# Kernel tuning notes

Hardware: AMD Instinct MI355X
Metric: run time of the kernel (lower is better)

## Reference

```python
import jax, jax.numpy as jnp
import numpy as np

N_HEADS = 16
N_KV_HEADS = 4
HEAD_DIM = 128  # d_model // n_heads = 2048 // 16
ROPE_THETA = 10000.0


def _rope_cos_sin(T, D, dtype):
    inv_freq = 1.0 / (ROPE_THETA ** (jnp.arange(0, D, 2, dtype=jnp.float32) / D))
    t = jnp.arange(T, dtype=jnp.float32)
    freqs = jnp.outer(t, inv_freq)               # [T, D/2]
    emb = jnp.concatenate([freqs, freqs], axis=-1)  # [T, D]
    return jnp.cos(emb).astype(dtype), jnp.sin(emb).astype(dtype)


def _rotate_half(x):
    x1, x2 = jnp.split(x, 2, axis=-1)
    return jnp.concatenate([-x2, x1], axis=-1)


def setup_inputs() -> dict:
    key = jax.random.key(0)
    k1, k2, k3, k4, k5 = jax.random.split(key, 5)
    B, T, C = 2, 2048, 2048
    H, KV, D = N_HEADS, N_KV_HEADS, HEAD_DIM
    s = 0.02
    return {
        "x": jax.random.normal(k1, (B, T, C), dtype=jnp.float32),
        "Wq": jax.random.normal(k2, (C, H * D), dtype=jnp.float32) * s,
        "Wk": jax.random.normal(k3, (C, KV * D), dtype=jnp.float32) * s,
        "Wv": jax.random.normal(k4, (C, KV * D), dtype=jnp.float32) * s,
        "Wo": jax.random.normal(k5, (H * D, C), dtype=jnp.float32) * s,
    }


def reference(x, Wq, Wk, Wv, Wo):
    B, T, C = x.shape
    H, KV, D = N_HEADS, N_KV_HEADS, HEAD_DIM
    G = H // KV
    scale = D ** -0.5

    q = (x @ Wq).reshape(B, T, H, D).transpose(0, 2, 1, 3)    # [B,H,T,D]
    k = (x @ Wk).reshape(B, T, KV, D).transpose(0, 2, 1, 3)   # [B,KV,T,D]
    v = (x @ Wv).reshape(B, T, KV, D).transpose(0, 2, 1, 3)   # [B,KV,T,D]

    cos, sin = _rope_cos_sin(T, D, x.dtype)  # [T,D] each, broadcasts over B,H
    q = q * cos + _rotate_half(q) * sin
    k = k * cos + _rotate_half(k) * sin

    # repeat_interleave kv heads to match query heads
    k = jnp.repeat(k, G, axis=1)  # [B,H,T,D]
    v = jnp.repeat(v, G, axis=1)  # [B,H,T,D]

    scores = jnp.einsum('bhqd,bhkd->bhqk', q, k) * scale  # [B,H,T,T]
    causal = jnp.tril(jnp.ones((T, T), dtype=bool))
    scores = jnp.where(causal, scores, jnp.finfo(scores.dtype).min)
    attn = jax.nn.softmax(scores, axis=-1)

    out = jnp.einsum('bhqk,bhkd->bhqd', attn, v)           # [B,H,T,D]
    out = out.transpose(0, 2, 1, 3).reshape(B, T, H * D)    # [B,T,C]
    return out @ Wo
```

## Files before the change

kernel.cpp:

```cpp
#include <hip/hip_runtime.h>
#include <cstdint>
#include <cstddef>

typedef __attribute__((ext_vector_type(4))) float f32x4;
typedef __attribute__((ext_vector_type(8))) short s16x8;
typedef __attribute__((ext_vector_type(4))) short s16x4;

#define B_  2
#define T_  2048
#define C_  2048
#define H_  16
#define KV_ 4
#define D_  128
#define M_  4096

static __device__ __forceinline__ float bf2f(ushort u){
  union { float f; uint32_t u; } x; x.u = ((uint32_t)u) << 16; return x.f;
}
static __device__ __forceinline__ ushort f2bf(float f){
  union { float f; uint32_t u; } x; x.f = f;
  uint32_t r = x.u + 0x7FFF + ((x.u >> 16) & 1);
  return (ushort)(r >> 16);
}

static __device__ __forceinline__ void gl_lds16(const ushort* g, ushort* s){
  __builtin_amdgcn_global_load_lds((const __attribute__((address_space(1))) void*)g,
                                   (__attribute__((address_space(3))) void*)s, 16, 0, 0);
}

__global__ void cvt_f32_bf16(const float* __restrict__ in, ushort* __restrict__ out, int n4){
  int idx = blockIdx.x * blockDim.x + threadIdx.x;
  int stride = gridDim.x * blockDim.x;
  for (int i = idx; i < n4; i += stride){
    float4 v = ((const float4*)in)[i];
    s16x4 o;
    o[0] = (short)f2bf(v.x); o[1] = (short)f2bf(v.y);
    o[2] = (short)f2bf(v.z); o[3] = (short)f2bf(v.w);
    ((s16x4*)out)[i] = o;
  }
}

__global__ void transpose_cvt(const float* __restrict__ W, ushort* __restrict__ Wt, int K, int N){
  __shared__ float tile[32][33];
  int n0 = blockIdx.x * 32, k0 = blockIdx.y * 32;
  int tx = threadIdx.x, ty = threadIdx.y;
  #pragma unroll
  for (int r = 0; r < 4; r++)
    tile[ty + 8*r][tx] = W[(size_t)(k0 + ty + 8*r) * N + n0 + tx];
  __syncthreads();
  #pragma unroll
  for (int r = 0; r < 4; r++)
    Wt[(size_t)(n0 + ty + 8*r) * K + k0 + tx] = f2bf(tile[tx][ty + 8*r]);
}

template<int MODE>
__global__ __launch_bounds__(512)
void gemm_deep(const ushort* __restrict__ A, const ushort* __restrict__ Bt,
               void* __restrict__ C0, void* __restrict__ C1, void* __restrict__ C2,
               int N, int Kd, int nbx){
  __shared__ __align__(16) ushort Abuf[4][8192];
  __shared__ __align__(16) ushort Bbuf[4][8192];
  int tid = threadIdx.x, w = tid >> 6, l = tid & 63;
  int l15 = l & 15, l4 = l >> 4;

  int cpx = gridDim.x >> 3;
  int logical = (blockIdx.x & 7) * cpx + (blockIdx.x >> 3);
  int bx = logical % nbx, by = logical / nbx;
  int rblk = by * 128, cblk = bx * 128;
  int wm = w & 1, wn = w >> 1;

  int sr = tid >> 3;
  int sc = ((tid & 7) * 8) ^ ((sr & 7) << 3);
  const ushort* gA = A  + (size_t)(rblk + sr) * Kd + sc;
  const ushort* gB = Bt + (size_t)(cblk + sr) * Kd + sc;
  size_t rowK = (size_t)64 * Kd;
  int wb = w * 512;

  auto stage = [&](int t){
    int bsel = t & 3; int koff = t * 64;
    gl_lds16(gA + koff,        &Abuf[bsel][wb]);
    gl_lds16(gA + rowK + koff, &Abuf[bsel][4096 + wb]);
    gl_lds16(gB + koff,        &Bbuf[bsel][wb]);
    gl_lds16(gB + rowK + koff, &Bbuf[bsel][4096 + wb]);
  };

  int arow = wm * 64 + l15;
  int brow = wn * 32 + l15;
  int kx0 = (l4 * 8) ^ ((l15 & 7) << 3);
  int kx1 = (32 + l4 * 8) ^ ((l15 & 7) << 3);

  f32x4 acc[4][2] = {};

  auto phase = [&](int t, int dostage, int vm){
    const ushort* Ab = Abuf[t & 3];
    const ushort* Bb = Bbuf[t & 3];
    s16x8 a[4][2], b[2][2];
    #pragma unroll
    for (int m = 0; m < 4; m++){
      a[m][0] = *(const s16x8*)(Ab + (arow + m*16) * 64 + kx0);
      a[m][1] = *(const s16x8*)(Ab + (arow + m*16) * 64 + kx1);
    }
    #pragma unroll
    for (int n = 0; n < 2; n++){
      b[n][0] = *(const s16x8*)(Bb + (brow + n*16) * 64 + kx0);
      b[n][1] = *(const s16x8*)(Bb + (brow + n*16) * 64 + kx1);
    }
    if (dostage) stage(t + 3);
    if (vm == 8)      { asm volatile("s_waitcnt vmcnt(8)" ::: "memory"); }
    else if (vm == 4) { asm volatile("s_waitcnt vmcnt(4)" ::: "memory"); }
    else if (vm == 0) { asm volatile("s_waitcnt vmcnt(0)" ::: "memory"); }
    if (vm >= 0) __builtin_amdgcn_sched_barrier(0);
    __builtin_amdgcn_s_barrier();
    asm volatile("s_waitcnt lgkmcnt(0)" ::: "memory");
    __builtin_amdgcn_sched_barrier(0);
    __builtin_amdgcn_s_setprio(1);
    #pragma unroll
    for (int m = 0; m < 4; m++)
      #pragma unroll
      for (int n = 0; n < 2; n++){
        acc[m][n] = __builtin_amdgcn_mfma_f32_16x16x32_bf16(a[m][0], b[n][0], acc[m][n], 0, 0, 0);
        acc[m][n] = __builtin_amdgcn_mfma_f32_16x16x32_bf16(a[m][1], b[n][1], acc[m][n], 0, 0, 0);
      }
    __builtin_amdgcn_s_setprio(0);
    __builtin_amdgcn_s_barrier();
  };

  stage(0); stage(1); stage(2);
  asm volatile("s_waitcnt vmcnt(8)" ::: "memory");
  __builtin_amdgcn_s_barrier();

  int nt = Kd >> 6;
  for (int t = 0; t < nt - 3; ++t) phase(t, 1, 8);
  phase(nt - 3, 0, 4);
  phase(nt - 2, 0, 0);
  phase(nt - 1, 0, -1);

  #pragma unroll
  for (int m = 0; m < 4; m++){
    #pragma unroll
    for (int n = 0; n < 2; n++){
      #pragma unroll
      for (int j = 0; j < 4; j++){
        int row = rblk + wm*64 + m*16 + l4*4 + j;
        int col = cblk + wn*32 + n*16 + l15;
        float v = acc[m][n][j];
        if (MODE == 0){
          ((float*)C0)[(size_t)row * N + col] = v;
        } else {
          int t = row & (T_ - 1), bb = row >> 11;
          ushort bv = f2bf(v);
          if (cblk < 2048){
            int hh = col >> 7, d = col & 127;
            ((ushort*)C0)[(((size_t)(bb * H_ + hh)) * T_ + t) * D_ + d] = bv;
          } else if (cblk < 2560){
            int c2 = col - 2048;
            int hh = c2 >> 7, d = c2 & 127;
            ((ushort*)C1)[(((size_t)(bb * KV_ + hh)) * T_ + t) * D_ + d] = bv;
          } else {
            int c2 = col - 2560;
            int hh = c2 >> 7, d = c2 & 127;
            ((ushort*)C2)[(((size_t)(bb * KV_ + hh)) * D_ + d) * T_ + t] = bv;
          }
        }
      }
    }
  }
}

__global__ __launch_bounds__(256)
void rope_inplace2(ushort* __restrict__ X, float scale){
  int tr = threadIdx.x >> 4;
  int j  = threadIdx.x & 15;
  int t  = blockIdx.x * 16 + tr;
  int bh = blockIdx.y;
  ushort* row = X + ((size_t)bh * T_ + t) * D_;
  s16x4 lo = *(const s16x4*)(row + j*4);
  s16x4 hi = *(const s16x4*)(row + 64 + j*4);
  s16x4 olo, ohi;
  #pragma unroll
  for (int i = 0; i < 4; i++){
    int d = j*4 + i;
    float invf = exp2f(-(float)d * 0.2076205059304602f);
    float s, c;
    __sincosf((float)t * invf, &s, &c);
    float q1 = bf2f((ushort)lo[i]);
    float q2 = bf2f((ushort)hi[i]);
    olo[i] = (short)f2bf((q1 * c - q2 * s) * scale);
    ohi[i] = (short)f2bf((q2 * c + q1 * s) * scale);
  }
  *(s16x4*)(row + j*4) = olo;
  *(s16x4*)(row + 64 + j*4) = ohi;
}

__global__ __launch_bounds__(512, 4)
void attn_kernel4(const ushort* __restrict__ Q, const ushort* __restrict__ Kc,
                  const ushort* __restrict__ Vt, ushort* __restrict__ O){
  __shared__ __align__(16) ushort Ks[64 * 128];
  __shared__ __align__(16) ushort Vs[128 * 64];
  __shared__ __align__(16) ushort Ps[8 * 16 * 64];
  int bid = blockIdx.x;
  int i  = bid >> 3;
  int qt = (i < 32) ? (63 - i) : (i - 32);
  int sub = bid & 7;
  int b = sub >> 2, kvh = sub & 3;
  int tid = threadIdx.x, w = tid >> 6, l = tid & 63;
  int l15 = l & 15, l4 = l >> 4;
  int sw3 = (l15 & 7) << 3;
  int q0 = qt * 32;
  int hq = kvh * 4 + (w >> 1);
  int qrow0 = q0 + (w & 1) * 16;
  int qrow = qrow0 + l15;

  s16x8 qf[4];
  const ushort* qbase = Q + (((size_t)(b * H_ + hq)) * T_ + qrow) * D_;
  #pragma unroll
  for (int kk = 0; kk < 4; kk++)
    qf[kk] = *(const s16x8*)(qbase + kk * 32 + l4 * 8);

  f32x4 oacc[8] = {};
  float mrun = -1e30f;
  float rsum = 0.f;
  const float THR = 11.5415603f;
  ushort* Pw = Ps + w * (16 * 64) + l15 * 64;

  const ushort* kbase = Kc + ((size_t)(b * KV_ + kvh)) * T_ * D_;
  const ushort* vbase = Vt + ((size_t)(b * KV_ + kvh)) * D_ * T_;
  int jmax = (q0 + 31) >> 6;

  int kr0 = tid >> 4, kcb = tid & 15;
  int vd0 = tid >> 3, vtb = tid & 7;
  int ksoff = kr0 * 128 + ((kcb * 8) ^ ((kr0 & 7) << 3));
  int vsoff = vd0 * 64  + ((vtb * 8) ^ ((vd0 & 7) << 3));
  const ushort* kg = kbase + (size_t)kr0 * D_ + kcb * 8;
  const ushort* vg = vbase + (size_t)vd0 * T_ + vtb * 8;

  s16x8 kreg0, kreg1, vreg0, vreg1;
  kreg0 = *(const s16x8*)(kg);
  kreg1 = *(const s16x8*)(kg + (size_t)32 * D_);
  vreg0 = *(const s16x8*)(vg);
  vreg1 = *(const s16x8*)(vg + (size_t)64 * T_);

  for (int jt = 0; jt <= jmax; jt++){
    __syncthreads();
    *(s16x8*)(Ks + ksoff)            = kreg0;
    *(s16x8*)(Ks + ksoff + 32 * 128) = kreg1;
    *(s16x8*)(Vs + vsoff)            = vreg0;
    *(s16x8*)(Vs + vsoff + 64 * 64)  = vreg1;
    __syncthreads();
    if (jt < jmax){
      int k1 = (jt + 1) * 64;
      kreg0 = *(const s16x8*)(kg + (size_t)k1 * D_);
      kreg1 = *(const s16x8*)(kg + (size_t)(k1 + 32) * D_);
      vreg0 = *(const s16x8*)(vg + k1);
      vreg1 = *(const s16x8*)(vg + (size_t)64 * T_ + k1);
    }
    int k0 = jt * 64;

    f32x4 sacc[4] = {};
    __builtin_amdgcn_s_setprio(1);
    #pragma unroll
    for (int kk = 0; kk < 4; kk++){
      #pragma unroll
      for (int n = 0; n < 4; n++){
        s16x8 kf = *(const s16x8*)(Ks + (16*n + l15) * 128 + ((kk*32 + l4*8) ^ sw3));
        sacc[n] = __builtin_amdgcn_mfma_f32_16x16x32_bf16(kf, qf[kk], sacc[n], 0, 0, 0);
      }
    }
    __builtin_amdgcn_s_setprio(0);
    if (jt == jmax){
      #pragma unroll
      for (int n = 0; n < 4; n++)
        #pragma unroll
        for (int j = 0; j < 4; j++){
          int kcol = k0 + 16*n + 4*l4 + j;
          if (kcol > qrow) sacc[n][j] = -1e30f;
        }
    }
    float mloc = -1e30f;
    #pragma unroll
    for (int n = 0; n < 4; n++)
      #pragma unroll
      for (int j = 0; j < 4; j++)
        mloc = fmaxf(mloc, sacc[n][j]);
    if (__any((int)(mloc > mrun + THR))){
      float m2 = fmaxf(mloc, __shfl_xor(mloc, 16));
      m2 = fmaxf(m2, __shfl_xor(m2, 32));
      float mnew = fmaxf(mrun, m2);
      float alpha = exp2f(mrun - mnew);
      mrun = mnew;
      rsum *= alpha;
      #pragma unroll
      for (int n8 = 0; n8 < 8; n8++)
        #pragma unroll
        for (int j = 0; j < 4; j++)
          oacc[n8][j] *= alpha;
    }
    #pragma unroll
    for (int n = 0; n < 4; n++){
      s16x4 pk;
      #pragma unroll
      for (int j = 0; j < 4; j++){
        float p = exp2f(sacc[n][j] - mrun);
        rsum += p;
        pk[j] = (short)f2bf(p);
      }
      *(s16x4*)(Pw + ((16*n + 4*l4) ^ sw3)) = pk;
    }
    __builtin_amdgcn_s_setprio(1);
    #pragma unroll
    for (int kk = 0; kk < 2; kk++){
      s16x8 pf = *(const s16x8*)(Pw + ((kk*32 + l4*8) ^ sw3));
      #pragma unroll
      for (int n8 = 0; n8 < 8; n8++){
        s16x8 vf = *(const s16x8*)(Vs + (16*n8 + l15) * 64 + ((kk*32 + l4*8) ^ sw3));
        oacc[n8] = __builtin_amdgcn_mfma_f32_16x16x32_bf16(vf, pf, oacc[n8], 0, 0, 0);
      }
    }
    __builtin_amdgcn_s_setprio(0);
  }

  rsum += __shfl_xor(rsum, 16);
  rsum += __shfl_xor(rsum, 32);
  float inv = 1.f / rsum;
  ushort* obase = O + ((size_t)(b * T_ + qrow)) * C_ + hq * D_ + 4*l4;
  #pragma unroll
  for (int n8 = 0; n8 < 8; n8++){
    s16x4 ov;
    #pragma unroll
    for (int j = 0; j < 4; j++)
      ov[j] = (short)f2bf(oacc[n8][j] * inv);
    *(s16x4*)(obase + 16*n8) = ov;
  }
}

extern "C" void kernel_launch(void* const* d_in, const int* in_sizes, int n_in,
                              void* d_out, int out_size, void* d_ws, size_t ws_size,
                              hipStream_t stream){
  const float* x  = (const float*)d_in[0];
  const float* Wq = (const float*)d_in[1];
  const float* Wk = (const float*)d_in[2];
  const float* Wv = (const float*)d_in[3];
  const float* Wo = (const float*)d_in[4];
  float* out = (float*)d_out;

  char* ws = (char*)d_ws;
  size_t off = 0;
  auto alloc = [&](size_t bytes)->void*{
    void* p = ws + off; off += (bytes + 255) & ~(size_t)255; return p;
  };
  ushort* xb   = (ushort*)alloc((size_t)M_ * C_ * 2);
  ushort* Wcat = (ushort*)alloc((size_t)3072 * 2048 * 2);
  ushort* Wot  = (ushort*)alloc((size_t)2048 * 2048 * 2);
  ushort* Qb   = (ushort*)alloc((size_t)B_ * H_ * T_ * D_ * 2);
  ushort* Kb   = (ushort*)alloc((size_t)B_ * KV_ * T_ * D_ * 2);
  ushort* Vtb  = (ushort*)alloc((size_t)B_ * KV_ * T_ * D_ * 2);
  ushort* Ob   = (ushort*)alloc((size_t)M_ * C_ * 2);

  cvt_f32_bf16<<<2048, 256, 0, stream>>>(x, xb, M_ * C_ / 4);
  transpose_cvt<<<dim3(64, 64), dim3(32, 8), 0, stream>>>(Wq, Wcat, 2048, 2048);
  transpose_cvt<<<dim3(16, 64), dim3(32, 8), 0, stream>>>(Wk, Wcat + (size_t)2048*2048, 2048, 512);
  transpose_cvt<<<dim3(16, 64), dim3(32, 8), 0, stream>>>(Wv, Wcat + (size_t)2560*2048, 2048, 512);
  transpose_cvt<<<dim3(64, 64), dim3(32, 8), 0, stream>>>(Wo, Wot, 2048, 2048);

  gemm_deep<1><<<768, 512, 0, stream>>>(xb, Wcat, Qb, Kb, Vtb, 3072, 2048, 24);

  rope_inplace2<<<dim3(T_/16, B_ * H_),  256, 0, stream>>>(Qb, 0.08838834764831845f * 1.4426950408889634f);
  rope_inplace2<<<dim3(T_/16, B_ * KV_), 256, 0, stream>>>(Kb, 1.0f);

  attn_kernel4<<<512, 512, 0, stream>>>(Qb, Kb, Vtb, Ob);

  gemm_deep<0><<<512, 512, 0, stream>>>(Ob, Wot, out, nullptr, nullptr, 2048, 2048, 16);
}
```

Baseline: 223.0 us.

## Merge weight transposes and RoPE launches, drop trailing GEMM phase barrier

Four weight transpose launches are merged into one kernel that picks its source by block index, and the Q and K RoPE launches become a single kernel. This removes launch overhead and the gaps between small kernels. Inside the GEMM main loop the second s_barrier per phase is removed and the remaining barrier moves after the LDS waitcnt, with the loop kept rolled. Dropping that barrier risks a race on the 4-deep LDS buffer ring, because a stage write could overlap reads of the same slot. The QKV scatter now branches on the column instead of the block's start column, which gives the same result for 128-aligned blocks.

```diff
diff --git a/kernel.cpp b/kernel.cpp
--- a/kernel.cpp
+++ b/kernel.cpp
@@ -40,9 +40,17 @@
   }
 }
 
-__global__ void transpose_cvt(const float* __restrict__ W, ushort* __restrict__ Wt, int K, int N){
+__global__ void transpose_all(const float* __restrict__ Wq, const float* __restrict__ Wk,
+                              const float* __restrict__ Wv, const float* __restrict__ Wo,
+                              ushort* __restrict__ Wcat, ushort* __restrict__ Wot){
   __shared__ float tile[32][33];
-  int n0 = blockIdx.x * 32, k0 = blockIdx.y * 32;
+  int bx = blockIdx.x;
+  const float* W; ushort* Wt; int N; int n0;
+  if (bx < 64)      { W = Wq; Wt = Wcat;                          N = 2048; n0 = bx * 32; }
+  else if (bx < 80) { W = Wk; Wt = Wcat + (size_t)2048 * 2048;    N = 512;  n0 = (bx - 64) * 32; }
+  else if (bx < 96) { W = Wv; Wt = Wcat + (size_t)2560 * 2048;    N = 512;  n0 = (bx - 80) * 32; }
+  else              { W = Wo; Wt = Wot;                           N = 2048; n0 = (bx - 96) * 32; }
+  int k0 = blockIdx.y * 32;
   int tx = threadIdx.x, ty = threadIdx.y;
   #pragma unroll
   for (int r = 0; r < 4; r++)
@@ -50,7 +58,7 @@
   __syncthreads();
   #pragma unroll
   for (int r = 0; r < 4; r++)
-    Wt[(size_t)(n0 + ty + 8*r) * K + k0 + tx] = f2bf(tile[tx][ty + 8*r]);
+    Wt[(size_t)(n0 + ty + 8*r) * 2048 + k0 + tx] = f2bf(tile[tx][ty + 8*r]);
 }
 
 template<int MODE>
@@ -109,10 +117,9 @@
     if (vm == 8)      { asm volatile("s_waitcnt vmcnt(8)" ::: "memory"); }
     else if (vm == 4) { asm volatile("s_waitcnt vmcnt(4)" ::: "memory"); }
     else if (vm == 0) { asm volatile("s_waitcnt vmcnt(0)" ::: "memory"); }
-    if (vm >= 0) __builtin_amdgcn_sched_barrier(0);
-    __builtin_amdgcn_s_barrier();
     asm volatile("s_waitcnt lgkmcnt(0)" ::: "memory");
     __builtin_amdgcn_sched_barrier(0);
+    __builtin_amdgcn_s_barrier();
     __builtin_amdgcn_s_setprio(1);
     #pragma unroll
     for (int m = 0; m < 4; m++)
@@ -122,7 +129,6 @@
         acc[m][n] = __builtin_amdgcn_mfma_f32_16x16x32_bf16(a[m][1], b[n][1], acc[m][n], 0, 0, 0);
       }
     __builtin_amdgcn_s_setprio(0);
-    __builtin_amdgcn_s_barrier();
   };
 
   stage(0); stage(1); stage(2);
@@ -130,6 +136,7 @@
   __builtin_amdgcn_s_barrier();
 
   int nt = Kd >> 6;
+  #pragma unroll 1
   for (int t = 0; t < nt - 3; ++t) phase(t, 1, 8);
   phase(nt - 3, 0, 4);
   phase(nt - 2, 0, 0);
@@ -149,10 +156,10 @@
         } else {
           int t = row & (T_ - 1), bb = row >> 11;
           ushort bv = f2bf(v);
-          if (cblk < 2048){
+          if (col < 2048){
             int hh = col >> 7, d = col & 127;
             ((ushort*)C0)[(((size_t)(bb * H_ + hh)) * T_ + t) * D_ + d] = bv;
-          } else if (cblk < 2560){
+          } else if (col < 2560){
             int c2 = col - 2048;
             int hh = c2 >> 7, d = c2 & 127;
             ((ushort*)C1)[(((size_t)(bb * KV_ + hh)) * T_ + t) * D_ + d] = bv;
@@ -168,11 +175,14 @@
 }
 
 __global__ __launch_bounds__(256)
-void rope_inplace2(ushort* __restrict__ X, float scale){
+void rope_all(ushort* __restrict__ Qb, ushort* __restrict__ Kb, float sq){
+  int y = blockIdx.y;
+  ushort* X; int bh; float scale;
+  if (y < B_ * H_){ X = Qb; bh = y;           scale = sq;  }
+  else            { X = Kb; bh = y - B_ * H_; scale = 1.f; }
   int tr = threadIdx.x >> 4;
   int j  = threadIdx.x & 15;
   int t  = blockIdx.x * 16 + tr;
-  int bh = blockIdx.y;
   ushort* row = X + ((size_t)bh * T_ + t) * D_;
   s16x4 lo = *(const s16x4*)(row + j*4);
   s16x4 hi = *(const s16x4*)(row + 64 + j*4);
@@ -357,15 +367,12 @@
   ushort* Ob   = (ushort*)alloc((size_t)M_ * C_ * 2);
 
   cvt_f32_bf16<<<2048, 256, 0, stream>>>(x, xb, M_ * C_ / 4);
-  transpose_cvt<<<dim3(64, 64), dim3(32, 8), 0, stream>>>(Wq, Wcat, 2048, 2048);
-  transpose_cvt<<<dim3(16, 64), dim3(32, 8), 0, stream>>>(Wk, Wcat + (size_t)2048*2048, 2048, 512);
-  transpose_cvt<<<dim3(16, 64), dim3(32, 8), 0, stream>>>(Wv, Wcat + (size_t)2560*2048, 2048, 512);
-  transpose_cvt<<<dim3(64, 64), dim3(32, 8), 0, stream>>>(Wo, Wot, 2048, 2048);
+  transpose_all<<<dim3(160, 64), dim3(32, 8), 0, stream>>>(Wq, Wk, Wv, Wo, Wcat, Wot);
 
   gemm_deep<1><<<768, 512, 0, stream>>>(xb, Wcat, Qb, Kb, Vtb, 3072, 2048, 24);
 
-  rope_inplace2<<<dim3(T_/16, B_ * H_),  256, 0, stream>>>(Qb, 0.08838834764831845f * 1.4426950408889634f);
-  rope_inplace2<<<dim3(T_/16, B_ * KV_), 256, 0, stream>>>(Kb, 1.0f);
+  rope_all<<<dim3(T_/16, B_ * (H_ + KV_)), 256, 0, stream>>>(
+      Qb, Kb, 0.08838834764831845f * 1.4426950408889634f);
 
   attn_kernel4<<<512, 512, 0, stream>>>(Qb, Kb, Vtb, Ob);
 
```

Result: faster. 211.0 us (-5.4%).
